# Kernel tuning notes

Measured on AMD Instinct MI355X. Metric: run time of the kernel, lower is better.

The kernel has to match this reference:

```python
import jax, jax.numpy as jnp
import numpy as np

N_ATOMS = 100000
N_CRYSTALS = 2048
ATOM_FEA_DIM = 64
NUM_HEAD = 32


def setup_inputs() -> dict:
    key = jax.random.key(0)
    k1, k2, k3, k4, k5 = jax.random.split(key, 5)
    atom_feas = jax.random.normal(k1, (N_ATOMS, ATOM_FEA_DIM), dtype=jnp.float32)
    Wk = jax.random.normal(k2, (ATOM_FEA_DIM, NUM_HEAD), dtype=jnp.float32) / jnp.sqrt(ATOM_FEA_DIM).astype(jnp.float32)
    bk = jax.random.normal(k3, (NUM_HEAD,), dtype=jnp.float32) * 0.01
    atomic_numbers = jax.random.randint(k4, (N_ATOMS,), 0, 94, dtype=jnp.int64 if jax.config.jax_enable_x64 else jnp.int32)
    atom_owner = jnp.sort(jax.random.randint(k5, (N_ATOMS,), 0, N_CRYSTALS, dtype=jnp.int64 if jax.config.jax_enable_x64 else jnp.int32))
    return {"atom_feas": atom_feas, "Wk": Wk, "bk": bk,
            "atomic_numbers": atomic_numbers, "atom_owner": atom_owner}


def reference(atom_feas, Wk, bk, atomic_numbers, atom_owner):
    # per-atom attention logits: [N, H]
    w = atom_feas @ Wk + bk
    # numerically-stable per-graph softmax over the ragged atom axis
    seg_max = jax.ops.segment_max(w, atom_owner, num_segments=N_CRYSTALS)  # [G, H]
    e = jnp.exp(w - seg_max[atom_owner])                                   # [N, H]
    seg_sum = jax.ops.segment_sum(e, atom_owner, num_segments=N_CRYSTALS)  # [G, H]
    p = e / seg_sum[atom_owner]                                            # [N, H]
    # per-graph atom_fea.T @ weight: outer product per atom, segment-summed -> [G, D, H]
    crystal = jax.ops.segment_sum(atom_feas[:, :, None] * p[:, None, :],
                                  atom_owner, num_segments=N_CRYSTALS)
    return crystal.reshape(N_CRYSTALS, ATOM_FEA_DIM * NUM_HEAD)
```

## Files before the change

### kernel.cpp

```cpp
#include <hip/hip_runtime.h>

#define NC 2048
#define D 64
#define H 32

typedef __fp16 h2 __attribute__((ext_vector_type(2)));
typedef unsigned int u32;

#if __has_builtin(__builtin_amdgcn_fdot2)
#define FDOT2(a, b, c) __builtin_amdgcn_fdot2((a), (b), (c), false)
#else
#define FDOT2(a, b, c) ((c) + (float)(a)[0] * (float)(b)[0] + (float)(a)[1] * (float)(b)[1])
#endif
#define BC2(u) __builtin_bit_cast(h2, (u))

__global__ void bounds_kernel(const int* __restrict__ owner,
                              int* __restrict__ bounds, int n) {
    int i = blockIdx.x * blockDim.x + threadIdx.x;
    if (i >= n) return;
    int o  = owner[i];
    int op = (i == 0) ? -1 : owner[i - 1];
    for (int g = op + 1; g <= o; ++g) bounds[g] = i;
    if (i == n - 1)
        for (int g = o + 1; g <= NC; ++g) bounds[g] = n;
}

__global__ __launch_bounds__(128)
void crystal_kernel(
    const float* __restrict__ atom_feas,
    const float* __restrict__ Wk,
    const float* __restrict__ bk,
    const int* __restrict__ bounds,
    float* __restrict__ out,
    int n)
{
    __shared__ float part[64][33];
    __shared__ __align__(16) u32 stage[2][2][8][32];
    __shared__ float lds_pad[1800];

    const int g    = blockIdx.x;
    const int tid  = threadIdx.x;
    const int lane = tid & 63;
    const int wv   = tid >> 6;
    const int h    = lane & 31;
    const int dg   = lane >> 5;
    const int d0   = dg * 32;

    h2 wkh[16];
    #pragma unroll
    for (int j = 0; j < 16; ++j) {
        const float wa = Wk[(d0 + 2 * j) * H + h];
        const float wb = Wk[(d0 + 2 * j + 1) * H + h];
        wkh[j] = __builtin_amdgcn_cvt_pkrtz(wa, wb);
    }
    const float bkv = bk[h];

    const int s   = bounds[g];
    const int e   = bounds[g + 1];
    const int per = (e - s + 1) >> 1;
    const int a0  = s + wv * per;
    const int ae  = min(a0 + per, e);

    float acc[32];
    #pragma unroll
    for (int j = 0; j < 32; ++j) acc[j] = 0.f;
    float es = 0.f;

    if (a0 < ae) {
        const int nchunk = (ae - a0 + 7) >> 3;
        const int maxf4  = n * 16 - 1;
        const float4* af4 = (const float4*)atom_feas;

        int cb = a0;
        float4 r0 = af4[min(cb * 16 + lane,      maxf4)];
        float4 r1 = af4[min(cb * 16 + lane + 64, maxf4)];

        for (int c = 0; c < nchunk; ++c) {
            {
                uint2* sw = (uint2*)stage[wv][c & 1];
                const h2 p0 = __builtin_amdgcn_cvt_pkrtz(r0.x, r0.y);
                const h2 p1 = __builtin_amdgcn_cvt_pkrtz(r0.z, r0.w);
                const h2 p2 = __builtin_amdgcn_cvt_pkrtz(r1.x, r1.y);
                const h2 p3 = __builtin_amdgcn_cvt_pkrtz(r1.z, r1.w);
                uint2 w0, w1;
                w0.x = __builtin_bit_cast(u32, p0); w0.y = __builtin_bit_cast(u32, p1);
                w1.x = __builtin_bit_cast(u32, p2); w1.y = __builtin_bit_cast(u32, p3);
                const int slot = lane & 15, arow = lane >> 4;
                sw[arow * 16 + slot]       = w0;
                sw[(arow + 4) * 16 + slot] = w1;
            }
            const int nb = cb + 8;
            if (c + 1 < nchunk) {
                r0 = af4[min(nb * 16 + lane,      maxf4)];
                r1 = af4[min(nb * 16 + lane + 64, maxf4)];
            }

            const uint4* srbase = (const uint4*)stage[wv][c & 1];
            #pragma unroll 2
            for (int i = 0; i < 8; ++i) {
                const int aa = cb + i;
                const uint4* sr = srbase + i * 8 + dg * 4;
                const uint4 x0 = sr[0], x1 = sr[1], x2 = sr[2], x3 = sr[3];

                float q0 = 0.f, q1 = 0.f, q2 = 0.f, q3 = 0.f;
                q0 = FDOT2(BC2(x0.x), wkh[0],  q0);
                q0 = FDOT2(BC2(x0.y), wkh[1],  q0);
                q0 = FDOT2(BC2(x0.z), wkh[2],  q0);
                q0 = FDOT2(BC2(x0.w), wkh[3],  q0);
                q1 = FDOT2(BC2(x1.x), wkh[4],  q1);
                q1 = FDOT2(BC2(x1.y), wkh[5],  q1);
                q1 = FDOT2(BC2(x1.z), wkh[6],  q1);
                q1 = FDOT2(BC2(x1.w), wkh[7],  q1);
                q2 = FDOT2(BC2(x2.x), wkh[8],  q2);
                q2 = FDOT2(BC2(x2.y), wkh[9],  q2);
                q2 = FDOT2(BC2(x2.z), wkh[10], q2);
                q2 = FDOT2(BC2(x2.w), wkh[11], q2);
                q3 = FDOT2(BC2(x3.x), wkh[12], q3);
                q3 = FDOT2(BC2(x3.y), wkh[13], q3);
                q3 = FDOT2(BC2(x3.z), wkh[14], q3);
                q3 = FDOT2(BC2(x3.w), wkh[15], q3);
                float wl = (q0 + q1) + (q2 + q3);
                wl += __shfl_xor(wl, 32, 64);
                const float p = (aa < ae) ? __expf(wl + bkv) : 0.f;
                es += p;

#define OUT2(U, j) { const h2 hh = BC2(U); \
                     acc[j]     += (float)hh[0] * p; \
                     acc[(j)+1] += (float)hh[1] * p; }
                OUT2(x0.x, 0)  OUT2(x0.y, 2)  OUT2(x0.z, 4)  OUT2(x0.w, 6)
                OUT2(x1.x, 8)  OUT2(x1.y, 10) OUT2(x1.z, 12) OUT2(x1.w, 14)
                OUT2(x2.x, 16) OUT2(x2.y, 18) OUT2(x2.z, 20) OUT2(x2.w, 22)
                OUT2(x3.x, 24) OUT2(x3.y, 26) OUT2(x3.z, 28) OUT2(x3.w, 30)
#undef OUT2
            }
            cb = nb;
        }
    }

    if (e < s) lds_pad[tid] = es;

    if (wv == 1) {
        #pragma unroll
        for (int j = 0; j < 32; ++j) part[lane][j] = acc[j];
        part[lane][32] = es;
    }
    __syncthreads();
    if (wv == 0) {
        #pragma unroll
        for (int j = 0; j < 32; ++j) acc[j] += part[lane][j];
        es += part[lane][32];
        const float inv = (es > 0.f) ? 1.0f / es : 0.f;
        float* og = out + (size_t)g * (D * H);
        #pragma unroll
        for (int j = 0; j < 32; ++j)
            og[(d0 + j) * H + h] = acc[j] * inv;
    }
}

#define CHUNK 64
__global__ __launch_bounds__(256) void fused_kernel(
    const float* __restrict__ atom_feas,
    const float* __restrict__ Wk,
    const float* __restrict__ bk,
    const int* __restrict__ owner,
    float* __restrict__ out,
    int n_atoms)
{
    __shared__ float fea_lds[CHUNK * D];
    __shared__ float w_lds[CHUNK * H];
    __shared__ float wk_lds[D * H];
    __shared__ float bk_lds[H];

    const int g   = blockIdx.x;
    const int tid = threadIdx.x;
    const int h   = tid & 31;
    const int grp = tid >> 5;

    for (int i = tid; i < D * H; i += 256) wk_lds[i] = Wk[i];
    if (tid < H) bk_lds[tid] = bk[tid];

    int lo = 0, hi = n_atoms;
    while (lo < hi) { int mid = (lo + hi) >> 1; if (owner[mid] < g) lo = mid + 1; else hi = mid; }
    const int seg_start = lo;
    hi = n_atoms;
    while (lo < hi) { int mid = (lo + hi) >> 1; if (owner[mid] < g + 1) lo = mid + 1; else hi = mid; }
    const int seg_end = lo;

    float acc[8];
    #pragma unroll
    for (int j = 0; j < 8; ++j) acc[j] = 0.f;
    float ps = 0.f;

    __syncthreads();

    for (int base = seg_start; base < seg_end; base += CHUNK) {
        const int na = min(CHUNK, seg_end - base);
        {
            const int nf4 = na * (D / 4);
            const float4* src = (const float4*)(atom_feas + (size_t)base * D);
            float4* dst = (float4*)fea_lds;
            for (int i = tid; i < nf4; i += 256) dst[i] = src[i];
        }
        __syncthreads();

        for (int pi = tid; pi < na * H; pi += 256) {
            const int aa = pi >> 5;
            const int hh = pi & 31;
            const float* fr = fea_lds + aa * D;
            float wvl = bk_lds[hh];
            #pragma unroll
            for (int k = 0; k < D; k += 4) {
                float4 f = *(const float4*)(fr + k);
                wvl += f.x * wk_lds[(k + 0) * H + hh];
                wvl += f.y * wk_lds[(k + 1) * H + hh];
                wvl += f.z * wk_lds[(k + 2) * H + hh];
                wvl += f.w * wk_lds[(k + 3) * H + hh];
            }
            w_lds[pi] = __expf(wvl);
        }
        __syncthreads();

        for (int aa = 0; aa < na; ++aa) {
            const float p = w_lds[aa * H + h];
            ps += p;
            const float* f = fea_lds + aa * D + grp * 8;
            #pragma unroll
            for (int j = 0; j < 8; ++j) acc[j] += f[j] * p;
        }
        __syncthreads();
    }

    const float inv = (ps > 0.f) ? 1.0f / ps : 0.f;
    float* og = out + (size_t)g * (D * H);
    #pragma unroll
    for (int j = 0; j < 8; ++j) og[(grp * 8 + j) * H + h] = acc[j] * inv;
}

extern "C" void kernel_launch(void* const* d_in, const int* in_sizes, int n_in,
                              void* d_out, int out_size, void* d_ws, size_t ws_size,
                              hipStream_t stream) {
    const float* atom_feas = (const float*)d_in[0];
    const float* Wk        = (const float*)d_in[1];
    const float* bk        = (const float*)d_in[2];
    const int*   owner     = (const int*)d_in[4];
    const int n_atoms = in_sizes[4];
    float* out = (float*)d_out;

    if (ws_size >= (NC + 1) * sizeof(int)) {
        int* bounds = (int*)d_ws;
        bounds_kernel<<<(n_atoms + 255) / 256, 256, 0, stream>>>(owner, bounds, n_atoms);
        crystal_kernel<<<NC, 128, 0, stream>>>(atom_feas, Wk, bk, bounds, out, n_atoms);
    } else {
        fused_kernel<<<NC, 256, 0, stream>>>(atom_feas, Wk, bk, owner, out, n_atoms);
    }
}
```

Before: 34.44 us.

## Split logits and exp into a precompute kernel and stream fp16 weights into readout

Replaces the separate bounds kernel with a logits kernel. It builds the bounds array, computes each atom's 32 logits from LDS-staged features and Wk in fp32, and writes exp(logit) as packed fp16 to the workspace. The readout kernel then loads these precomputed weights alongside the features instead of doing per-atom fdot2 dot products, a cross-lane shuffle and exp. This takes the logit work off the per-crystal critical path, and removing the padding LDS array may allow more blocks per CU. In exchange, atom_feas is read twice, an extra fp16 buffer is written and read, and exp values stored in fp16 can lose precision or overflow for large logits.

```diff
diff --git a/kernel.cpp b/kernel.cpp
--- a/kernel.cpp
+++ b/kernel.cpp
@@ -3,40 +3,94 @@
 #define NC 2048
 #define D 64
 #define H 32
+#define FPAD 68
 
 typedef __fp16 h2 __attribute__((ext_vector_type(2)));
 typedef unsigned int u32;
 
-#if __has_builtin(__builtin_amdgcn_fdot2)
-#define FDOT2(a, b, c) __builtin_amdgcn_fdot2((a), (b), (c), false)
-#else
-#define FDOT2(a, b, c) ((c) + (float)(a)[0] * (float)(b)[0] + (float)(a)[1] * (float)(b)[1])
-#endif
-#define BC2(u) __builtin_bit_cast(h2, (u))
-
-__global__ void bounds_kernel(const int* __restrict__ owner,
-                              int* __restrict__ bounds, int n) {
-    int i = blockIdx.x * blockDim.x + threadIdx.x;
-    if (i >= n) return;
-    int o  = owner[i];
-    int op = (i == 0) ? -1 : owner[i - 1];
-    for (int g = op + 1; g <= o; ++g) bounds[g] = i;
-    if (i == n - 1)
-        for (int g = o + 1; g <= NC; ++g) bounds[g] = n;
-}
-
-__global__ __launch_bounds__(128)
-void crystal_kernel(
+#define BCH(u) __builtin_bit_cast(h2, (u))
+
+__global__ __launch_bounds__(256) void logits_kernel(
     const float* __restrict__ atom_feas,
     const float* __restrict__ Wk,
     const float* __restrict__ bk,
+    const int* __restrict__ owner,
+    u32* __restrict__ e16,
+    int* __restrict__ bounds,
+    int n)
+{
+    __shared__ float fea_lds[64 * FPAD];
+    __shared__ float wk_lds[D * H];
+    __shared__ float bk_lds[H];
+
+    const int tid  = threadIdx.x;
+    const int base = blockIdx.x * 64;
+    const int na   = min(64, n - base);
+
+    const int gi = blockIdx.x * 256 + tid;
+    if (gi < n) {
+        const int o  = owner[gi];
+        const int op = (gi == 0) ? -1 : owner[gi - 1];
+        for (int g = op + 1; g <= o; ++g) bounds[g] = gi;
+        if (gi == n - 1)
+            for (int g = o + 1; g <= NC; ++g) bounds[g] = n;
+    }
+
+    for (int i = tid; i < D * H; i += 256) wk_lds[i] = Wk[i];
+    if (tid < H) bk_lds[tid] = bk[tid];
+
+    {
+        const float4* src = (const float4*)(atom_feas + (size_t)base * D);
+        const int nf4 = na * (D / 4);
+        for (int i = tid; i < nf4; i += 256) {
+            const int a = i >> 4, c2 = i & 15;
+            *(float4*)(fea_lds + a * FPAD + c2 * 4) = src[i];
+        }
+    }
+    __syncthreads();
+
+    const int a  = tid >> 2;
+    const int h0 = (tid & 3) * 8;
+    if (a < na) {
+        float acc[8];
+        #pragma unroll
+        for (int j = 0; j < 8; ++j) acc[j] = bk_lds[h0 + j];
+
+        const float* fr = fea_lds + a * FPAD;
+        #pragma unroll
+        for (int k = 0; k < D; k += 4) {
+            const float4 f = *(const float4*)(fr + k);
+            #pragma unroll
+            for (int r = 0; r < 4; ++r) {
+                const float fv = (&f.x)[r];
+                const float4 w0 = *(const float4*)(wk_lds + (k + r) * H + h0);
+                const float4 w1 = *(const float4*)(wk_lds + (k + r) * H + h0 + 4);
+                acc[0] += fv * w0.x; acc[1] += fv * w0.y;
+                acc[2] += fv * w0.z; acc[3] += fv * w0.w;
+                acc[4] += fv * w1.x; acc[5] += fv * w1.y;
+                acc[6] += fv * w1.z; acc[7] += fv * w1.w;
+            }
+        }
+        uint4 pk;
+        pk.x = __builtin_bit_cast(u32, __builtin_amdgcn_cvt_pkrtz(__expf(acc[0]), __expf(acc[1])));
+        pk.y = __builtin_bit_cast(u32, __builtin_amdgcn_cvt_pkrtz(__expf(acc[2]), __expf(acc[3])));
+        pk.z = __builtin_bit_cast(u32, __builtin_amdgcn_cvt_pkrtz(__expf(acc[4]), __expf(acc[5])));
+        pk.w = __builtin_bit_cast(u32, __builtin_amdgcn_cvt_pkrtz(__expf(acc[6]), __expf(acc[7])));
+        *(uint4*)(e16 + (size_t)(base + a) * 16 + (tid & 3) * 4) = pk;
+    }
+}
+
+__global__ __launch_bounds__(128)
+void readout_kernel(
+    const float* __restrict__ atom_feas,
+    const u32* __restrict__ e16,
     const int* __restrict__ bounds,
     float* __restrict__ out,
     int n)
 {
+    __shared__ __align__(16) u32 stage[2][2][8][32];
+    __shared__ __align__(8)  uint2 estage[2][2][64];
     __shared__ float part[64][33];
-    __shared__ __align__(16) u32 stage[2][2][8][32];
-    __shared__ float lds_pad[1800];
 
     const int g    = blockIdx.x;
     const int tid  = threadIdx.x;
@@ -46,15 +100,6 @@
     const int dg   = lane >> 5;
     const int d0   = dg * 32;
 
-    h2 wkh[16];
-    #pragma unroll
-    for (int j = 0; j < 16; ++j) {
-        const float wa = Wk[(d0 + 2 * j) * H + h];
-        const float wb = Wk[(d0 + 2 * j + 1) * H + h];
-        wkh[j] = __builtin_amdgcn_cvt_pkrtz(wa, wb);
-    }
-    const float bkv = bk[h];
-
     const int s   = bounds[g];
     const int e   = bounds[g + 1];
     const int per = (e - s + 1) >> 1;
@@ -69,11 +114,14 @@
     if (a0 < ae) {
         const int nchunk = (ae - a0 + 7) >> 3;
         const int maxf4  = n * 16 - 1;
+        const int maxe2  = n * 8 - 1;
         const float4* af4 = (const float4*)atom_feas;
+        const uint2*  e2  = (const uint2*)e16;
 
         int cb = a0;
         float4 r0 = af4[min(cb * 16 + lane,      maxf4)];
         float4 r1 = af4[min(cb * 16 + lane + 64, maxf4)];
+        uint2  eu = e2 [min(cb * 8  + lane,      maxe2)];
 
         for (int c = 0; c < nchunk; ++c) {
             {
@@ -88,56 +136,45 @@
                 const int slot = lane & 15, arow = lane >> 4;
                 sw[arow * 16 + slot]       = w0;
                 sw[(arow + 4) * 16 + slot] = w1;
+                estage[wv][c & 1][lane] = eu;
             }
             const int nb = cb + 8;
             if (c + 1 < nchunk) {
                 r0 = af4[min(nb * 16 + lane,      maxf4)];
                 r1 = af4[min(nb * 16 + lane + 64, maxf4)];
+                eu = e2 [min(nb * 8  + lane,      maxe2)];
             }
 
             const uint4* srbase = (const uint4*)stage[wv][c & 1];
+            const u32*   ep     = (const u32*)estage[wv][c & 1];
             #pragma unroll 2
             for (int i = 0; i < 8; ++i) {
                 const int aa = cb + i;
+                const u32 ew = ep[i * 16 + (h >> 1)];
+                const u32 sel = (h & 1) ? (ew >> 16) : (ew & 0xffffu);
+                float p = (float)__builtin_bit_cast(__fp16, (unsigned short)sel);
+                p = (aa < ae) ? p : 0.f;
+                es += p;
+
                 const uint4* sr = srbase + i * 8 + dg * 4;
                 const uint4 x0 = sr[0], x1 = sr[1], x2 = sr[2], x3 = sr[3];
-
-                float q0 = 0.f, q1 = 0.f, q2 = 0.f, q3 = 0.f;
-                q0 = FDOT2(BC2(x0.x), wkh[0],  q0);
-                q0 = FDOT2(BC2(x0.y), wkh[1],  q0);
-                q0 = FDOT2(BC2(x0.z), wkh[2],  q0);
-                q0 = FDOT2(BC2(x0.w), wkh[3],  q0);
-                q1 = FDOT2(BC2(x1.x), wkh[4],  q1);
-                q1 = FDOT2(BC2(x1.y), wkh[5],  q1);
-                q1 = FDOT2(BC2(x1.z), wkh[6],  q1);
-                q1 = FDOT2(BC2(x1.w), wkh[7],  q1);
-                q2 = FDOT2(BC2(x2.x), wkh[8],  q2);
-                q2 = FDOT2(BC2(x2.y), wkh[9],  q2);
-                q2 = FDOT2(BC2(x2.z), wkh[10], q2);
-                q2 = FDOT2(BC2(x2.w), wkh[11], q2);
-                q3 = FDOT2(BC2(x3.x), wkh[12], q3);
-                q3 = FDOT2(BC2(x3.y), wkh[13], q3);
-                q3 = FDOT2(BC2(x3.z), wkh[14], q3);
-                q3 = FDOT2(BC2(x3.w), wkh[15], q3);
-                float wl = (q0 + q1) + (q2 + q3);
-                wl += __shfl_xor(wl, 32, 64);
-                const float p = (aa < ae) ? __expf(wl + bkv) : 0.f;
-                es += p;
-
-#define OUT2(U, j) { const h2 hh = BC2(U); \
-                     acc[j]     += (float)hh[0] * p; \
-                     acc[(j)+1] += (float)hh[1] * p; }
-                OUT2(x0.x, 0)  OUT2(x0.y, 2)  OUT2(x0.z, 4)  OUT2(x0.w, 6)
-                OUT2(x1.x, 8)  OUT2(x1.y, 10) OUT2(x1.z, 12) OUT2(x1.w, 14)
-                OUT2(x2.x, 16) OUT2(x2.y, 18) OUT2(x2.z, 20) OUT2(x2.w, 22)
-                OUT2(x3.x, 24) OUT2(x3.y, 26) OUT2(x3.z, 28) OUT2(x3.w, 30)
-#undef OUT2
+#define OUTQ(Y, base)                                     \
+                { const h2 ha = BCH(Y.x); const h2 hb = BCH(Y.y); \
+                  const h2 hc = BCH(Y.z); const h2 hd = BCH(Y.w); \
+                  acc[base + 0] += (float)ha[0] * p;              \
+                  acc[base + 1] += (float)ha[1] * p;              \
+                  acc[base + 2] += (float)hb[0] * p;              \
+                  acc[base + 3] += (float)hb[1] * p;              \
+                  acc[base + 4] += (float)hc[0] * p;              \
+                  acc[base + 5] += (float)hc[1] * p;              \
+                  acc[base + 6] += (float)hd[0] * p;              \
+                  acc[base + 7] += (float)hd[1] * p; }
+                OUTQ(x0, 0) OUTQ(x1, 8) OUTQ(x2, 16) OUTQ(x3, 24)
+#undef OUTQ
             }
             cb = nb;
         }
     }
-
-    if (e < s) lds_pad[tid] = es;
 
     if (wv == 1) {
         #pragma unroll
@@ -246,10 +283,18 @@
     const int n_atoms = in_sizes[4];
     float* out = (float*)d_out;
 
-    if (ws_size >= (NC + 1) * sizeof(int)) {
+    const size_t bounds_bytes = 16384;
+    const size_t e_bytes = (size_t)n_atoms * H * 2;
+
+    if (ws_size >= bounds_bytes + e_bytes) {
         int* bounds = (int*)d_ws;
-        bounds_kernel<<<(n_atoms + 255) / 256, 256, 0, stream>>>(owner, bounds, n_atoms);
-        crystal_kernel<<<NC, 128, 0, stream>>>(atom_feas, Wk, bk, bounds, out, n_atoms);
+        u32* e16    = (u32*)((char*)d_ws + bounds_bytes);
+
+        const int nb = (n_atoms + 63) / 64;
+        logits_kernel<<<nb, 256, 0, stream>>>(atom_feas, Wk, bk, owner,
+                                              e16, bounds, n_atoms);
+        readout_kernel<<<NC, 128, 0, stream>>>(atom_feas, e16, bounds,
+                                               out, n_atoms);
     } else {
         fused_kernel<<<NC, 256, 0, stream>>>(atom_feas, Wk, bk, owner, out, n_atoms);
     }
```

Measured after the change: 41.24 us. 19.8% more time.
